# Optimization experiments

Hardware: AMD Instinct MI355X
Metric: run time of the kernel (lower is better)

## Reference

```python
import jax, jax.numpy as jnp
import numpy as np
import math

M_BITS = 256


def setup_inputs() -> dict:
    key = jax.random.key(0)
    k1, k2, k3, k4, k5, k6 = jax.random.split(key, 6)
    B, N, D, MB, DH = 8, 2048, 1024, M_BITS, 128
    return {
        "Q": jax.random.normal(k1, (B, N, D), dtype=jnp.float32),
        "K": jax.random.normal(k2, (B, N, D), dtype=jnp.float32),
        "V": jax.random.normal(k3, (B, N, D), dtype=jnp.float32),
        "Wq": jax.random.normal(k4, (D, MB), dtype=jnp.float32) / math.sqrt(D),
        "Wk": jax.random.normal(k5, (D, MB), dtype=jnp.float32) / math.sqrt(D),
        "Wv": jax.random.normal(k6, (D, DH), dtype=jnp.float32) / math.sqrt(D),
    }


def reference(Q, K, V, Wq, Wk, Wv):
    # Boolean REWA encoding: project then hard-binarize (sign bits).
    # sim(q,k) = #matching bits = (s_q . s_k + m) / 2 with s = 2*bit - 1.
    m = Wq.shape[1]
    scale = 1.0 / math.sqrt(m)
    sq = jnp.where(jnp.einsum('bnd,dm->bnm', Q, Wq) > 0, 1.0, -1.0)  # [B,N,m]
    sk = jnp.where(jnp.einsum('bkd,dm->bkm', K, Wk) > 0, 1.0, -1.0)  # [B,M,m]
    dot = jnp.einsum('bnm,bkm->bnk', sq, sk)                         # [B,N,M]
    scores = 0.5 * (dot + m) * scale
    attn = jax.nn.softmax(scores, axis=-1)                           # [B,N,M]
    Vp = jnp.einsum('bkd,dh->bkh', V, Wv)                            # [B,M,d_head]
    out = jnp.einsum('bnk,bkh->bnh', attn, Vp)                       # [B,N,d_head]
    return out, attn
```

## Files before the change

kernel.cpp:

```cpp
#include <hip/hip_runtime.h>


typedef __attribute__((ext_vector_type(4))) float f32x4;
typedef __attribute__((ext_vector_type(8))) __bf16 bf16x8;

#define FLAG_CAP 32768
#define FLAG_TAU 2e-4f

__device__ inline unsigned short f2b(float x) {
    unsigned int u = __float_as_uint(x);
    return (unsigned short)((u + 0x7FFFu + ((u >> 16) & 1u)) >> 16);
}

__global__ __launch_bounds__(256) void prep_weights(
    const float* __restrict__ Wq, const float* __restrict__ Wk, const float* __restrict__ Wv,
    unsigned short* __restrict__ WqhT, unsigned short* __restrict__ WqlT,
    unsigned short* __restrict__ WkhT, unsigned short* __restrict__ WklT,
    unsigned short* __restrict__ WvhT, int* __restrict__ flag_count)
{
    if (blockIdx.x == 0 && threadIdx.x == 0) *flag_count = 0;
    int i = blockIdx.x * 256 + threadIdx.x;
    const float* src; unsigned short *dh, *dl; int cols, j;
    if (i < 262144)      { src = Wq; dh = WqhT; dl = WqlT; cols = 256; j = i; }
    else if (i < 524288) { src = Wk; dh = WkhT; dl = WklT; cols = 256; j = i - 262144; }
    else                 { src = Wv; dh = WvhT; dl = nullptr; cols = 128; j = i - 524288; }
    int d = j / cols, m = j % cols;
    float x = src[j];
    unsigned short h = f2b(x);
    dh[(size_t)m * 1024 + d] = h;
    if (dl) {
        float hf = __uint_as_float(((unsigned int)h) << 16);
        dl[(size_t)m * 1024 + d] = f2b(x - hf);
    }
}

__global__ __launch_bounds__(256) void proj_kernel(
    const float* __restrict__ Q, const float* __restrict__ K, const float* __restrict__ V,
    const unsigned short* __restrict__ WqhT, const unsigned short* __restrict__ WqlT,
    const unsigned short* __restrict__ WkhT, const unsigned short* __restrict__ WklT,
    const unsigned short* __restrict__ WvhT,
    unsigned short* __restrict__ Sq, unsigned short* __restrict__ Sk,
    unsigned short* __restrict__ VpT,
    int* __restrict__ flag_count, int* __restrict__ flags)
{
    const int z = blockIdx.z, y = blockIdx.y;
    if (z == 2 && y == 1) return;
    const int m0 = blockIdx.x * 64;
    const bool split = (z < 2);
    const int n0 = split ? y * 128 : 0;
    const float* src = (z == 0) ? Q : (z == 1) ? K : V;
    const unsigned short* BhT = (z == 0) ? WqhT : (z == 1) ? WkhT : WvhT;
    const unsigned short* BlT = (z == 0) ? WqlT : WklT;

    __shared__ __align__(16) unsigned short smem[15360];
    unsigned short* Ah = smem;
    unsigned short* Al = smem + 2560;
    unsigned short* Bh = smem + 5120;
    unsigned short* Bl = smem + 10240;

    const int tid = threadIdx.x;
    const int wid = tid >> 6, lane = tid & 63;
    const int lr = lane & 15, lg = lane >> 4;

    f32x4 acc[8];
    #pragma unroll
    for (int t = 0; t < 8; ++t) acc[t] = f32x4{0.f, 0.f, 0.f, 0.f};

    for (int ks = 0; ks < 32; ++ks) {
        const int k0 = ks * 32;
        __syncthreads();
        {
            const int row = tid >> 2, quad = tid & 3;
            const float* p = src + (size_t)(m0 + row) * 1024 + k0 + quad * 8;
            float4 v0 = *(const float4*)p;
            float4 v1 = *(const float4*)(p + 4);
            float xs[8] = {v0.x, v0.y, v0.z, v0.w, v1.x, v1.y, v1.z, v1.w};
            unsigned short hs[8], ls[8];
            #pragma unroll
            for (int i = 0; i < 8; ++i) {
                unsigned short h = f2b(xs[i]);
                float hf = __uint_as_float(((unsigned int)h) << 16);
                hs[i] = h;
                ls[i] = f2b(xs[i] - hf);
            }
            *(uint4*)(Ah + row * 40 + quad * 8) = *(const uint4*)hs;
            if (split) *(uint4*)(Al + row * 40 + quad * 8) = *(const uint4*)ls;
        }
        {
            const int row = tid >> 1, half = tid & 1;
            const unsigned short* ph = BhT + (size_t)(n0 + row) * 1024 + k0 + half * 16;
            uint4 b0 = *(const uint4*)ph;
            uint4 b1 = *(const uint4*)(ph + 8);
            *(uint4*)(Bh + row * 40 + half * 16) = b0;
            *(uint4*)(Bh + row * 40 + half * 16 + 8) = b1;
            if (split) {
                const unsigned short* pl = BlT + (size_t)(n0 + row) * 1024 + k0 + half * 16;
                uint4 c0 = *(const uint4*)pl;
                uint4 c1 = *(const uint4*)(pl + 8);
                *(uint4*)(Bl + row * 40 + half * 16) = c0;
                *(uint4*)(Bl + row * 40 + half * 16 + 8) = c1;
            }
        }
        __syncthreads();
        const bf16x8 a_h = *(const bf16x8*)(Ah + (wid * 16 + lr) * 40 + lg * 8);
        bf16x8 a_l;
        if (split) a_l = *(const bf16x8*)(Al + (wid * 16 + lr) * 40 + lg * 8);
        #pragma unroll
        for (int t = 0; t < 8; ++t) {
            const bf16x8 b_h = *(const bf16x8*)(Bh + (t * 16 + lr) * 40 + lg * 8);
            acc[t] = __builtin_amdgcn_mfma_f32_16x16x32_bf16(a_h, b_h, acc[t], 0, 0, 0);
            if (split) {
                const bf16x8 b_l = *(const bf16x8*)(Bl + (t * 16 + lr) * 40 + lg * 8);
                acc[t] = __builtin_amdgcn_mfma_f32_16x16x32_bf16(a_h, b_l, acc[t], 0, 0, 0);
                acc[t] = __builtin_amdgcn_mfma_f32_16x16x32_bf16(a_l, b_h, acc[t], 0, 0, 0);
            }
        }
    }

    if (z < 2) {
        unsigned short* dst = (z == 0) ? Sq : Sk;
        const int whichbit = z << 22;
        #pragma unroll
        for (int t = 0; t < 8; ++t)
            #pragma unroll
            for (int j = 0; j < 4; ++j) {
                const int row = m0 + wid * 16 + 4 * lg + j;
                const int col = n0 + t * 16 + lr;
                const float zv = acc[t][j];
                dst[(size_t)row * 256 + col] =
                    (zv > 0.f) ? (unsigned short)0x3F80 : (unsigned short)0xBF80;
                if (__builtin_fabsf(zv) < FLAG_TAU) {
                    int slot = atomicAdd(flag_count, 1);
                    if (slot < FLAG_CAP) flags[slot] = whichbit | (row << 8) | col;
                }
            }
    } else {
        __syncthreads();
        unsigned short* tp = smem;
        #pragma unroll
        for (int t = 0; t < 8; ++t)
            #pragma unroll
            for (int j = 0; j < 4; ++j) {
                const int h = t * 16 + lr;
                const int key = wid * 16 + 4 * lg + j;
                tp[h * 72 + key] = f2b(acc[t][j]);
            }
        __syncthreads();
        const int b = m0 >> 11, key0 = m0 & 2047;
        const int h = tid >> 1, half = tid & 1;
        const unsigned short* sp = tp + h * 72 + half * 32;
        unsigned short* gp = VpT + (size_t)(b * 128 + h) * 2048 + key0 + half * 32;
        #pragma unroll
        for (int i = 0; i < 4; ++i)
            *(uint4*)(gp + i * 8) = *(const uint4*)(sp + i * 8);
    }
}

__global__ __launch_bounds__(256) void fixup_kernel(
    const float* __restrict__ Q, const float* __restrict__ K,
    const float* __restrict__ Wq, const float* __restrict__ Wk,
    unsigned short* __restrict__ Sq, unsigned short* __restrict__ Sk,
    const int* __restrict__ flag_count, const int* __restrict__ flags)
{
    const int nflags = min(*flag_count, FLAG_CAP);
    const int wave = (int)(blockIdx.x * 256 + threadIdx.x) >> 6;
    const int lane = threadIdx.x & 63;
    const int nwaves = gridDim.x * 4;
    for (int i = wave; i < nflags; i += nwaves) {
        const int enc = flags[i];
        const int which = enc >> 22;
        const int row = (enc >> 8) & 0x3FFF;
        const int col = enc & 255;
        const float* srow = (which ? K : Q) + (size_t)row * 1024;
        const float* W = (which ? Wk : Wq) + col;
        double accd = 0.0;
        #pragma unroll 4
        for (int d = lane; d < 1024; d += 64)
            accd += (double)srow[d] * (double)W[(size_t)d * 256];
        #pragma unroll
        for (int off = 32; off; off >>= 1) accd += __shfl_xor(accd, off);
        if (lane == 0)
            (which ? Sk : Sq)[(size_t)row * 256 + col] =
                (accd > 0.0) ? (unsigned short)0x3F80 : (unsigned short)0xBF80;
    }
}

__global__ __launch_bounds__(256) void attn_kernel(
    const unsigned short* __restrict__ Sq, const unsigned short* __restrict__ Sk,
    const unsigned short* __restrict__ VpT,
    float* __restrict__ attn, float* __restrict__ out, float* __restrict__ rowsum)
{
    const int b = blockIdx.y;
    const int q0 = blockIdx.x * 64;
    const int tid = threadIdx.x;
    const int wid = tid >> 6, lane = tid & 63;
    const int lr = lane & 15, lg = lane >> 4;

    __shared__ __align__(16) unsigned short sk_lds[32][264];
    __shared__ __align__(16) unsigned short vpt_lds[128][40];
    __shared__ __align__(16) unsigned short e_lds[4][16][40];

    uint4 sqf[8];
    {
        const unsigned short* p =
            Sq + (size_t)(b * 2048 + q0 + wid * 16 + lr) * 256 + lg * 8;
        #pragma unroll
        for (int s = 0; s < 8; ++s) sqf[s] = *(const uint4*)(p + s * 32);
    }

    f32x4 oacc[8];
    #pragma unroll
    for (int t = 0; t < 8; ++t) oacc[t] = f32x4{0.f, 0.f, 0.f, 0.f};
    float racc[4] = {0.f, 0.f, 0.f, 0.f};

    float* attn_row_base = attn + (size_t)(b * 2048 + q0 + wid * 16 + 4 * lg) * 2048;

    for (int kt = 0; kt < 64; ++kt) {
        const int kt0 = kt * 32;
        __syncthreads();
        {
            const int row = tid >> 3, chunk = tid & 7;
            const unsigned short* p = Sk + (size_t)(b * 2048 + kt0 + row) * 256 + chunk * 32;
            uint4 v0 = *(const uint4*)(p);
            uint4 v1 = *(const uint4*)(p + 8);
            uint4 v2 = *(const uint4*)(p + 16);
            uint4 v3 = *(const uint4*)(p + 24);
            unsigned short* q = &sk_lds[row][chunk * 32];
            *(uint4*)(q) = v0; *(uint4*)(q + 8) = v1;
            *(uint4*)(q + 16) = v2; *(uint4*)(q + 24) = v3;
        }
        {
            const int h = tid >> 1, half = tid & 1;
            const unsigned short* p = VpT + (size_t)(b * 128 + h) * 2048 + kt0 + half * 16;
            uint4 v0 = *(const uint4*)(p);
            uint4 v1 = *(const uint4*)(p + 8);
            unsigned short* q = &vpt_lds[h][half * 16];
            *(uint4*)(q) = v0; *(uint4*)(q + 8) = v1;
        }
        __syncthreads();

        f32x4 dacc[2];
        dacc[0] = f32x4{0.f, 0.f, 0.f, 0.f};
        dacc[1] = f32x4{0.f, 0.f, 0.f, 0.f};
        #pragma unroll
        for (int s = 0; s < 8; ++s) {
            const bf16x8 a = *(const bf16x8*)(&sqf[s]);
            #pragma unroll
            for (int t2 = 0; t2 < 2; ++t2) {
                const bf16x8 bk = *(const bf16x8*)(&sk_lds[t2 * 16 + lr][s * 32 + lg * 8]);
                dacc[t2] = __builtin_amdgcn_mfma_f32_16x16x32_bf16(a, bk, dacc[t2], 0, 0, 0);
            }
        }
        #pragma unroll
        for (int t2 = 0; t2 < 2; ++t2)
            #pragma unroll
            for (int j = 0; j < 4; ++j) {
                float e = __expf((dacc[t2][j] + 256.0f) * 0.03125f);
                racc[j] += e;
                attn_row_base[(size_t)j * 2048 + kt0 + t2 * 16 + lr] = e;
                e_lds[wid][4 * lg + j][t2 * 16 + lr] = f2b(e);
            }
        const bf16x8 ea = *(const bf16x8*)(&e_lds[wid][lr][lg * 8]);
        #pragma unroll
        for (int t = 0; t < 8; ++t) {
            const bf16x8 vb = *(const bf16x8*)(&vpt_lds[t * 16 + lr][lg * 8]);
            oacc[t] = __builtin_amdgcn_mfma_f32_16x16x32_bf16(ea, vb, oacc[t], 0, 0, 0);
        }
    }

    #pragma unroll
    for (int j = 0; j < 4; ++j) {
        float v = racc[j];
        v += __shfl_xor(v, 1);
        v += __shfl_xor(v, 2);
        v += __shfl_xor(v, 4);
        v += __shfl_xor(v, 8);
        racc[j] = v;
    }
    if (lr == 0) {
        #pragma unroll
        for (int j = 0; j < 4; ++j)
            rowsum[b * 2048 + q0 + wid * 16 + 4 * lg + j] = racc[j];
    }
    #pragma unroll
    for (int t = 0; t < 8; ++t)
        #pragma unroll
        for (int j = 0; j < 4; ++j)
            out[(size_t)(b * 2048 + q0 + wid * 16 + 4 * lg + j) * 128 + t * 16 + lr] =
                oacc[t][j] / racc[j];
}

__global__ __launch_bounds__(256) void normalize_kernel(
    float* __restrict__ attn, const float* __restrict__ rowsum)
{
    const size_t idx4 = (size_t)blockIdx.x * 256 + threadIdx.x;
    const int row = (int)(idx4 >> 9);
    const float inv = 1.0f / rowsum[row];
    float4* p = (float4*)attn + idx4;
    float4 v = *p;
    v.x *= inv; v.y *= inv; v.z *= inv; v.w *= inv;
    *p = v;
}

extern "C" void kernel_launch(void* const* d_in, const int* in_sizes, int n_in,
                              void* d_out, int out_size, void* d_ws, size_t ws_size,
                              hipStream_t stream)
{
    const float* Q  = (const float*)d_in[0];
    const float* K  = (const float*)d_in[1];
    const float* V  = (const float*)d_in[2];
    const float* Wq = (const float*)d_in[3];
    const float* Wk = (const float*)d_in[4];
    const float* Wv = (const float*)d_in[5];

    unsigned short* ws   = (unsigned short*)d_ws;
    unsigned short* WqhT = ws;
    unsigned short* WqlT = WqhT + 262144;
    unsigned short* WkhT = WqlT + 262144;
    unsigned short* WklT = WkhT + 262144;
    unsigned short* WvhT = WklT + 262144;
    unsigned short* Sq   = WvhT + 131072;
    unsigned short* Sk   = Sq + 4194304;
    unsigned short* VpT  = Sk + 4194304;
    float* rowsum    = (float*)(VpT + 2097152);
    int* flag_count  = (int*)(rowsum + 16384);
    int* flags       = flag_count + 1;

    float* out  = (float*)d_out;
    float* attn = out + 2097152;

    prep_weights<<<2560, 256, 0, stream>>>(Wq, Wk, Wv, WqhT, WqlT, WkhT, WklT, WvhT,
                                           flag_count);
    proj_kernel<<<dim3(256, 2, 3), 256, 0, stream>>>(Q, K, V, WqhT, WqlT, WkhT, WklT, WvhT,
                                                     Sq, Sk, VpT, flag_count, flags);
    fixup_kernel<<<64, 256, 0, stream>>>(Q, K, Wq, Wk, Sq, Sk, flag_count, flags);
    attn_kernel<<<dim3(32, 8), 256, 0, stream>>>(Sq, Sk, VpT, attn, out, rowsum);
    normalize_kernel<<<32768, 256, 0, stream>>>(attn, rowsum);
}
```

Baseline: 552.7 us.

## Split attention over key dimension and software-pipeline projection GEMM loads

The attention kernel now splits the key range across a third grid dimension (up to 4 splits, depending on workspace size). This raises the block count from 256 so more CUs are occupied. Partial outputs and row sums go to workspace and are combined by a new finalize kernel, which costs extra traffic and a launch. The projection GEMM also prefetches the next k-tile into registers while the current one is computed, and uses the native bf16 conversion instead of manual rounding.

```diff
diff --git a/kernel.cpp b/kernel.cpp
--- a/kernel.cpp
+++ b/kernel.cpp
@@ -62,46 +62,54 @@
     const int wid = tid >> 6, lane = tid & 63;
     const int lr = lane & 15, lg = lane >> 4;
 
+    const int arow = tid >> 2, aquad = tid & 3;
+    const float* abase = src + (size_t)(m0 + arow) * 1024 + aquad * 8;
+    const int brow = tid >> 1, bhalf = tid & 1;
+    const unsigned short* bhbase = BhT + (size_t)(n0 + brow) * 1024 + bhalf * 16;
+    const unsigned short* blbase = BlT + (size_t)(n0 + brow) * 1024 + bhalf * 16;
+
+    float4 av0, av1;
+    uint4 bh0, bh1, bl0, bl1;
+
+    auto load_tile = [&](int k0) {
+        av0 = *(const float4*)(abase + k0);
+        av1 = *(const float4*)(abase + k0 + 4);
+        bh0 = *(const uint4*)(bhbase + k0);
+        bh1 = *(const uint4*)(bhbase + k0 + 8);
+        if (split) {
+            bl0 = *(const uint4*)(blbase + k0);
+            bl1 = *(const uint4*)(blbase + k0 + 8);
+        }
+    };
+    auto write_tile = [&]() {
+        float xs[8] = {av0.x, av0.y, av0.z, av0.w, av1.x, av1.y, av1.z, av1.w};
+        __bf16 hs[8], ls[8];
+        #pragma unroll
+        for (int i = 0; i < 8; ++i) {
+            __bf16 h = (__bf16)xs[i];
+            hs[i] = h;
+            ls[i] = (__bf16)(xs[i] - (float)h);
+        }
+        *(uint4*)(Ah + arow * 40 + aquad * 8) = *(const uint4*)hs;
+        if (split) *(uint4*)(Al + arow * 40 + aquad * 8) = *(const uint4*)ls;
+        *(uint4*)(Bh + brow * 40 + bhalf * 16) = bh0;
+        *(uint4*)(Bh + brow * 40 + bhalf * 16 + 8) = bh1;
+        if (split) {
+            *(uint4*)(Bl + brow * 40 + bhalf * 16) = bl0;
+            *(uint4*)(Bl + brow * 40 + bhalf * 16 + 8) = bl1;
+        }
+    };
+
     f32x4 acc[8];
     #pragma unroll
     for (int t = 0; t < 8; ++t) acc[t] = f32x4{0.f, 0.f, 0.f, 0.f};
 
+    load_tile(0);
+    write_tile();
+    __syncthreads();
+
     for (int ks = 0; ks < 32; ++ks) {
-        const int k0 = ks * 32;
-        __syncthreads();
-        {
-            const int row = tid >> 2, quad = tid & 3;
-            const float* p = src + (size_t)(m0 + row) * 1024 + k0 + quad * 8;
-            float4 v0 = *(const float4*)p;
-            float4 v1 = *(const float4*)(p + 4);
-            float xs[8] = {v0.x, v0.y, v0.z, v0.w, v1.x, v1.y, v1.z, v1.w};
-            unsigned short hs[8], ls[8];
-            #pragma unroll
-            for (int i = 0; i < 8; ++i) {
-                unsigned short h = f2b(xs[i]);
-                float hf = __uint_as_float(((unsigned int)h) << 16);
-                hs[i] = h;
-                ls[i] = f2b(xs[i] - hf);
-            }
-            *(uint4*)(Ah + row * 40 + quad * 8) = *(const uint4*)hs;
-            if (split) *(uint4*)(Al + row * 40 + quad * 8) = *(const uint4*)ls;
-        }
-        {
-            const int row = tid >> 1, half = tid & 1;
-            const unsigned short* ph = BhT + (size_t)(n0 + row) * 1024 + k0 + half * 16;
-            uint4 b0 = *(const uint4*)ph;
-            uint4 b1 = *(const uint4*)(ph + 8);
-            *(uint4*)(Bh + row * 40 + half * 16) = b0;
-            *(uint4*)(Bh + row * 40 + half * 16 + 8) = b1;
-            if (split) {
-                const unsigned short* pl = BlT + (size_t)(n0 + row) * 1024 + k0 + half * 16;
-                uint4 c0 = *(const uint4*)pl;
-                uint4 c1 = *(const uint4*)(pl + 8);
-                *(uint4*)(Bl + row * 40 + half * 16) = c0;
-                *(uint4*)(Bl + row * 40 + half * 16 + 8) = c1;
-            }
-        }
-        __syncthreads();
+        if (ks < 31) load_tile((ks + 1) * 32);
         const bf16x8 a_h = *(const bf16x8*)(Ah + (wid * 16 + lr) * 40 + lg * 8);
         bf16x8 a_l;
         if (split) a_l = *(const bf16x8*)(Al + (wid * 16 + lr) * 40 + lg * 8);
@@ -114,6 +122,11 @@
                 acc[t] = __builtin_amdgcn_mfma_f32_16x16x32_bf16(a_h, b_l, acc[t], 0, 0, 0);
                 acc[t] = __builtin_amdgcn_mfma_f32_16x16x32_bf16(a_l, b_h, acc[t], 0, 0, 0);
             }
+        }
+        if (ks < 31) {
+            __syncthreads();
+            write_tile();
+            __syncthreads();
         }
     }
 
@@ -188,10 +201,12 @@
 __global__ __launch_bounds__(256) void attn_kernel(
     const unsigned short* __restrict__ Sq, const unsigned short* __restrict__ Sk,
     const unsigned short* __restrict__ VpT,
-    float* __restrict__ attn, float* __restrict__ out, float* __restrict__ rowsum)
+    float* __restrict__ attn, float* __restrict__ out_or_part,
+    float* __restrict__ rowsum_part, int nsplit)
 {
     const int b = blockIdx.y;
     const int q0 = blockIdx.x * 64;
+    const int sp = blockIdx.z;
     const int tid = threadIdx.x;
     const int wid = tid >> 6, lane = tid & 63;
     const int lr = lane & 15, lg = lane >> 4;
@@ -215,7 +230,8 @@
 
     float* attn_row_base = attn + (size_t)(b * 2048 + q0 + wid * 16 + 4 * lg) * 2048;
 
-    for (int kt = 0; kt < 64; ++kt) {
+    const int tiles = 64 / nsplit;
+    for (int kt = sp * tiles; kt < sp * tiles + tiles; ++kt) {
         const int kt0 = kt * 32;
         __syncthreads();
         {
@@ -280,22 +296,52 @@
     if (lr == 0) {
         #pragma unroll
         for (int j = 0; j < 4; ++j)
-            rowsum[b * 2048 + q0 + wid * 16 + 4 * lg + j] = racc[j];
-    }
-    #pragma unroll
-    for (int t = 0; t < 8; ++t)
-        #pragma unroll
-        for (int j = 0; j < 4; ++j)
-            out[(size_t)(b * 2048 + q0 + wid * 16 + 4 * lg + j) * 128 + t * 16 + lr] =
-                oacc[t][j] / racc[j];
+            rowsum_part[sp * 16384 + b * 2048 + q0 + wid * 16 + 4 * lg + j] = racc[j];
+    }
+    if (nsplit == 1) {
+        #pragma unroll
+        for (int t = 0; t < 8; ++t)
+            #pragma unroll
+            for (int j = 0; j < 4; ++j)
+                out_or_part[(size_t)(b * 2048 + q0 + wid * 16 + 4 * lg + j) * 128
+                            + t * 16 + lr] = oacc[t][j] / racc[j];
+    } else {
+        #pragma unroll
+        for (int t = 0; t < 8; ++t)
+            #pragma unroll
+            for (int j = 0; j < 4; ++j)
+                out_or_part[((size_t)sp * 16384 + b * 2048 + q0 + wid * 16 + 4 * lg + j) * 128
+                            + t * 16 + lr] = oacc[t][j];
+    }
+}
+
+__global__ __launch_bounds__(256) void out_finalize(
+    float* __restrict__ out, const float* __restrict__ out_part,
+    const float* __restrict__ rowsum_part, int nsplit)
+{
+    const int idx4 = blockIdx.x * 256 + threadIdx.x;
+    const int row = idx4 >> 5;
+    float rs = 0.f;
+    for (int k = 0; k < nsplit; ++k) rs += rowsum_part[k * 16384 + row];
+    float4 s = {0.f, 0.f, 0.f, 0.f};
+    const float4* p = (const float4*)out_part;
+    for (int k = 0; k < nsplit; ++k) {
+        float4 v = p[(size_t)k * 524288 + idx4];
+        s.x += v.x; s.y += v.y; s.z += v.z; s.w += v.w;
+    }
+    const float inv = 1.0f / rs;
+    float4 r = {s.x * inv, s.y * inv, s.z * inv, s.w * inv};
+    ((float4*)out)[idx4] = r;
 }
 
 __global__ __launch_bounds__(256) void normalize_kernel(
-    float* __restrict__ attn, const float* __restrict__ rowsum)
+    float* __restrict__ attn, const float* __restrict__ rowsum_part, int nsplit)
 {
     const size_t idx4 = (size_t)blockIdx.x * 256 + threadIdx.x;
     const int row = (int)(idx4 >> 9);
-    const float inv = 1.0f / rowsum[row];
+    float rs = 0.f;
+    for (int k = 0; k < nsplit; ++k) rs += rowsum_part[k * 16384 + row];
+    const float inv = 1.0f / rs;
     float4* p = (float4*)attn + idx4;
     float4 v = *p;
     v.x *= inv; v.y *= inv; v.z *= inv; v.w *= inv;
@@ -322,9 +368,16 @@
     unsigned short* Sq   = WvhT + 131072;
     unsigned short* Sk   = Sq + 4194304;
     unsigned short* VpT  = Sk + 4194304;
-    float* rowsum    = (float*)(VpT + 2097152);
-    int* flag_count  = (int*)(rowsum + 16384);
-    int* flags       = flag_count + 1;
+    int* flag_count    = (int*)(VpT + 2097152);
+    int* flags         = flag_count + 1;
+    float* rowsum_part = (float*)(flags + FLAG_CAP);
+    const size_t fixed_bytes = (size_t)((char*)rowsum_part - (char*)d_ws);
+
+    int nsplit = 1;
+    if (ws_size >= fixed_bytes + 4u * (16384u + 2097152u) * sizeof(float)) nsplit = 4;
+    else if (ws_size >= fixed_bytes + 2u * (16384u + 2097152u) * sizeof(float)) nsplit = 2;
+
+    float* out_part = rowsum_part + (size_t)nsplit * 16384;
 
     float* out  = (float*)d_out;
     float* attn = out + 2097152;
@@ -334,6 +387,9 @@
     proj_kernel<<<dim3(256, 2, 3), 256, 0, stream>>>(Q, K, V, WqhT, WqlT, WkhT, WklT, WvhT,
                                                      Sq, Sk, VpT, flag_count, flags);
     fixup_kernel<<<64, 256, 0, stream>>>(Q, K, Wq, Wk, Sq, Sk, flag_count, flags);
-    attn_kernel<<<dim3(32, 8), 256, 0, stream>>>(Sq, Sk, VpT, attn, out, rowsum);
-    normalize_kernel<<<32768, 256, 0, stream>>>(attn, rowsum);
-}
+    attn_kernel<<<dim3(32, 8, nsplit), 256, 0, stream>>>(
+        Sq, Sk, VpT, attn, (nsplit == 1) ? out : out_part, rowsum_part, nsplit);
+    if (nsplit > 1)
+        out_finalize<<<2048, 256, 0, stream>>>(out, out_part, rowsum_part, nsplit);
+    normalize_kernel<<<32768, 256, 0, stream>>>(attn, rowsum_part, nsplit);
+}
```

Measured after the change: 482.5 us. -12.7%, faster.
